# Optimization experiments

Measured on AMD Instinct MI355X. Metric: run time of the kernel, lower is better.

The kernel has to match this reference:

```python
import jax, jax.numpy as jnp
import numpy as np

N, D, S, K = 4096, 256, 32, 4   # nodes, in_dim(=out_dim), subspace_dim, num_heads
ETA = 0.5
LAMBDA_SPARSE = 0.05
EDGE_P = 0.02  # graph density for the random adjacency mask


def setup_inputs() -> dict:
    key = jax.random.key(0)
    k1, k2, k3 = jax.random.split(key, 3)
    H = jax.random.normal(k1, (N, D), dtype=jnp.float32)
    # binary adjacency mask with self-loops, stored as float (matches torch usage)
    mask = (jax.random.uniform(k2, (N, N)) < EDGE_P).astype(jnp.float32)
    adj_mask = jnp.maximum(mask, jnp.eye(N, dtype=jnp.float32))
    # per-head orthonormal subspace bases U[k] = qr(randn(D,S)) -> [K, D, S]
    raw = jax.random.normal(k3, (K, D, S), dtype=jnp.float32)
    U, _ = jnp.linalg.qr(raw)
    log_precision = jnp.zeros((K, S), dtype=jnp.float32)
    threshold = jnp.full((D,), LAMBDA_SPARSE, dtype=jnp.float32)
    return {"H": H, "adj_mask": adj_mask, "U": U,
            "log_precision": log_precision, "threshold": threshold}


def reference(H, adj_mask, U, log_precision, threshold):
    s = U.shape[-1]
    inv_sqrt_s = 1.0 / jnp.sqrt(jnp.asarray(s, dtype=H.dtype))
    neg = (1.0 - adj_mask) * (-1e9)  # [N, N] additive mask

    # scan over heads keeps peak memory at one [N,N] score matrix at a time
    def head_step(agg, xs):
        Uk, lpk = xs                       # [D,S], [S]
        Z = H @ Uk                         # [N,S]  (= Zk^T in the torch code)
        Zs = Z * jnp.exp(lpk)              # precision-scaled
        scores = (Zs @ Z.T) * inv_sqrt_s + neg   # [N,N]
        alpha = jax.nn.softmax(scores, axis=-1)
        agg = agg + (alpha @ Z) @ Uk.T     # [N,D] == (Uk @ (Zk @ alpha^T))^T
        return agg, None

    agg, _ = jax.lax.scan(head_step, jnp.zeros_like(H), (U, log_precision))
    H_half = H + ETA * agg                 # in_dim == out_dim -> no proj

    # soft threshold
    H_out = jnp.sign(H_half) * jax.nn.relu(jnp.abs(H_half) - threshold[None, :])

    # orthogonality loss: sum_k ||Uk^T Uk - I||_F^2 + sum_{k<l} ||Uk^T Ul||_F^2
    C = jnp.einsum('kda,ldb->klab', U, U)  # [K,K,S,S] gram blocks (K,S small)
    Kh = U.shape[0]
    I = jnp.eye(s, dtype=U.dtype)
    diag_blocks = C[jnp.arange(Kh), jnp.arange(Kh)]          # [K,S,S]
    orth_loss = ((diag_blocks - I) ** 2).sum()
    upper = jnp.triu(jnp.ones((Kh, Kh), dtype=U.dtype), 1)[:, :, None, None]
    orth_loss = orth_loss + ((C ** 2) * upper).sum()
    return H_out, orth_loss
```

## Files before the change

kernel.cpp:

```cpp
#include <hip/hip_runtime.h>
#include <math.h>

constexpr int NN = 4096;
constexpr int DD = 256;
constexpr int SS = 32;
constexpr int KK = 4;
constexpr int MAXN = 192;
constexpr int SEGMAX = 96;
constexpr float ETA = 0.5f;
constexpr int RPB = 2;

#define MEMFENCE() __asm__ volatile("" ::: "memory")

typedef float nfloat4 __attribute__((ext_vector_type(4)));
__device__ __forceinline__ float4 ntload4(const float4* p) {
  nfloat4 v = __builtin_nontemporal_load((const nfloat4*)p);
  float4 r; r.x = v.x; r.y = v.y; r.z = v.z; r.w = v.w;
  return r;
}

__global__ __launch_bounds__(256) void prep_kernel(
    const float* __restrict__ H, const float* __restrict__ U,
    const float* __restrict__ lp, float* __restrict__ Z,
    float* __restrict__ elp, float* __restrict__ lossp) {
  __shared__ float Hl[16][DD];
  __shared__ float red[4];
  const int tid = threadIdx.x;

  if (blockIdx.x < 1024) {
    const int k = blockIdx.x & 3;
    const int n0 = (blockIdx.x >> 2) * 16;

    const float4* H4 = (const float4*)(H + (size_t)n0 * DD);
    float4* Hl4 = (float4*)&Hl[0][0];
    for (int i = tid; i < 16 * DD / 4; i += 256) Hl4[i] = H4[i];
    __syncthreads();

    const int s = tid & 31;
    const int n_l = (tid >> 5) & 7;
    const float* Uk = U + (size_t)k * DD * SS;
    float acc0 = 0.f, acc1 = 0.f;
#pragma unroll 4
    for (int dq = 0; dq < DD / 4; dq++) {
      const float4 h0 = Hl4[n_l * (DD / 4) + dq];
      const float4 h1 = Hl4[(n_l + 8) * (DD / 4) + dq];
      const float u0 = Uk[(4 * dq + 0) * SS + s];
      const float u1 = Uk[(4 * dq + 1) * SS + s];
      const float u2 = Uk[(4 * dq + 2) * SS + s];
      const float u3 = Uk[(4 * dq + 3) * SS + s];
      acc0 += h0.x * u0 + h0.y * u1 + h0.z * u2 + h0.w * u3;
      acc1 += h1.x * u0 + h1.y * u1 + h1.z * u2 + h1.w * u3;
    }
    Z[((size_t)k * NN + n0 + n_l) * SS + s] = acc0;
    Z[((size_t)k * NN + n0 + n_l + 8) * SS + s] = acc1;
  } else {
    const int pair = blockIdx.x - 1024;
    if (pair == 0 && tid < KK * SS) elp[tid] = expf(lp[tid]);
    const int pk[10] = {0, 0, 0, 0, 1, 1, 1, 2, 2, 3};
    const int pl[10] = {0, 1, 2, 3, 1, 2, 3, 2, 3, 3};
    const int k = pk[pair], l = pl[pair];
    const int b = tid & 31;
    const int a0 = tid >> 5;
    float4 acc = {0.f, 0.f, 0.f, 0.f};
    const float4* Uk4 = (const float4*)(U + (size_t)k * DD * SS);
    const float* Ul = U + (size_t)l * DD * SS;
    for (int d = 0; d < DD; d++) {
      const float ub = Ul[(size_t)d * SS + b];
      const float4 ua = Uk4[d * (SS / 4) + a0];
      acc.x += ua.x * ub; acc.y += ua.y * ub;
      acc.z += ua.z * ub; acc.w += ua.w * ub;
    }
    const int abase = 4 * a0;
    float cvx = acc.x - ((k == l && abase + 0 == b) ? 1.0f : 0.0f);
    float cvy = acc.y - ((k == l && abase + 1 == b) ? 1.0f : 0.0f);
    float cvz = acc.z - ((k == l && abase + 2 == b) ? 1.0f : 0.0f);
    float cvw = acc.w - ((k == l && abase + 3 == b) ? 1.0f : 0.0f);
    float tot = cvx * cvx + cvy * cvy + cvz * cvz + cvw * cvw;
#pragma unroll
    for (int off = 32; off >= 1; off >>= 1) tot += __shfl_xor(tot, off);
    if ((tid & 63) == 0) red[tid >> 6] = tot;
    __syncthreads();
    if (tid == 0) lossp[pair] = red[0] + red[1] + red[2] + red[3];
  }
}

__global__ __launch_bounds__(256, 8) void attn_epi(
    const float* __restrict__ mask, const float* __restrict__ Z,
    const float* __restrict__ elp, const float* __restrict__ lossp,
    const float* __restrict__ H, const float* __restrict__ U,
    const float* __restrict__ thr, float* __restrict__ Hout,
    float* __restrict__ loss) {
  const int tid = threadIdx.x;
  const int wv = tid >> 6;
  const int lane = tid & 63;
  const int bid = blockIdx.x;

  __shared__ int segn[RPB][4][SEGMAX];
  __shared__ int segc[RPB][4];
  __shared__ int nbr[RPB][MAXN];
  __shared__ float AOl[RPB][KK * SS];

  if (bid == 0 && tid == 0) {
    float t = 0.f;
#pragma unroll
    for (int i = 0; i < 10; i++) t += lossp[i];
    loss[0] = t;
  }

  const unsigned long long lt = (1ULL << lane) - 1ULL;

  {
    const float4* m4 = (const float4*)(mask + (size_t)(bid * RPB) * NN);
    const int base = wv * 256 + lane;
    float4 v[RPB][4];
#pragma unroll
    for (int r = 0; r < RPB; r++)
#pragma unroll
      for (int it = 0; it < 4; it++)
        v[r][it] = ntload4(&m4[(size_t)r * (NN / 4) + base + it * 64]);

#pragma unroll
    for (int r = 0; r < RPB; r++) {
      int cnt = 0;
#pragma unroll
      for (int it = 0; it < 4; it++) {
        const int i = base + it * 64;
        const float4 vv = v[r][it];
        unsigned long long bb;
        bb = __ballot(vv.x > 0.5f);
        if (vv.x > 0.5f) { const int p = cnt + (int)__popcll(bb & lt); if (p < SEGMAX) segn[r][wv][p] = 4 * i; }
        cnt += (int)__popcll(bb);
        bb = __ballot(vv.y > 0.5f);
        if (vv.y > 0.5f) { const int p = cnt + (int)__popcll(bb & lt); if (p < SEGMAX) segn[r][wv][p] = 4 * i + 1; }
        cnt += (int)__popcll(bb);
        bb = __ballot(vv.z > 0.5f);
        if (vv.z > 0.5f) { const int p = cnt + (int)__popcll(bb & lt); if (p < SEGMAX) segn[r][wv][p] = 4 * i + 2; }
        cnt += (int)__popcll(bb);
        bb = __ballot(vv.w > 0.5f);
        if (vv.w > 0.5f) { const int p = cnt + (int)__popcll(bb & lt); if (p < SEGMAX) segn[r][wv][p] = 4 * i + 3; }
        cnt += (int)__popcll(bb);
      }
      if (lane == 0) segc[r][wv] = min(cnt, SEGMAX);
    }
  }
  MEMFENCE();
  __syncthreads();

  int ctot[RPB];
#pragma unroll
  for (int r = 0; r < RPB; r++) {
    const int c0 = segc[r][0], c1 = segc[r][1];
    const int c2 = segc[r][2], c3 = segc[r][3];
    const int offs[4] = {0, c0, c0 + c1, c0 + c1 + c2};
    ctot[r] = min(c0 + c1 + c2 + c3, MAXN);
    const int myc = segc[r][wv];
    const int myoff = offs[wv];
    for (int i = lane; i < myc; i += 64) {
      const int p = myoff + i;
      if (p < MAXN) nbr[r][p] = segn[r][wv][i];
    }
  }
  MEMFENCE();
  __syncthreads();

  const int p_sub = lane >> 3;
  const int sq = lane & 7;
  const float inv_sqrt_s = 0.17677669529663687f;
  const int k = wv;
  const float* Zk = Z + (size_t)k * NN * SS;

#pragma unroll
  for (int r = 0; r < RPB; r++) {
    const int row = bid * RPB + r;
    const int c = ctot[r];
    const int* nb = &nbr[r][0];

    float4 q4;
    {
      const float4 a = ((const float4*)(Z + ((size_t)k * NN + row) * SS))[sq];
      const float4 e = ((const float4*)(elp + k * SS))[sq];
      q4.x = a.x * e.x; q4.y = a.y * e.y; q4.z = a.z * e.z; q4.w = a.w * e.w;
    }

    float m = -3.0e38f;
    float wsum = 0.f;
    float4 o4 = {0.f, 0.f, 0.f, 0.f};

    bool aA = p_sub < c, aB = (p_sub + 8) < c;
    float4 zA = {0.f, 0.f, 0.f, 0.f}, zB = {0.f, 0.f, 0.f, 0.f};
    if (aA) zA = ((const float4*)(Zk + (size_t)nb[p_sub] * SS))[sq];
    if (aB) zB = ((const float4*)(Zk + (size_t)nb[p_sub + 8] * SS))[sq];

    for (int p0 = 0; p0 < c; p0 += 16) {
      const int pa_n = p0 + 16 + p_sub;
      const int pb_n = pa_n + 8;
      const bool aA_n = pa_n < c, aB_n = pb_n < c;
      float4 zA_n = {0.f, 0.f, 0.f, 0.f}, zB_n = {0.f, 0.f, 0.f, 0.f};
      if (aA_n) zA_n = ((const float4*)(Zk + (size_t)nb[pa_n] * SS))[sq];
      if (aB_n) zB_n = ((const float4*)(Zk + (size_t)nb[pb_n] * SS))[sq];

      float dA = q4.x * zA.x + q4.y * zA.y + q4.z * zA.z + q4.w * zA.w;
      float dB = q4.x * zB.x + q4.y * zB.y + q4.z * zB.z + q4.w * zB.w;
      dA += __shfl_xor(dA, 1); dB += __shfl_xor(dB, 1);
      dA += __shfl_xor(dA, 2); dB += __shfl_xor(dB, 2);
      dA += __shfl_xor(dA, 4); dB += __shfl_xor(dB, 4);
      dA = aA ? dA * inv_sqrt_s : -3.0e38f;
      dB = aB ? dB * inv_sqrt_s : -3.0e38f;
      float cm = fmaxf(dA, dB);
      cm = fmaxf(cm, __shfl_xor(cm, 8));
      cm = fmaxf(cm, __shfl_xor(cm, 16));
      cm = fmaxf(cm, __shfl_xor(cm, 32));
      const float mn = fmaxf(m, cm);
      const float sc = __expf(m - mn);
      m = mn;
      const float wA = __expf(dA - m);
      const float wB = __expf(dB - m);
      o4.x = o4.x * sc + wA * zA.x + wB * zB.x;
      o4.y = o4.y * sc + wA * zA.y + wB * zB.y;
      o4.z = o4.z * sc + wA * zA.z + wB * zB.z;
      o4.w = o4.w * sc + wA * zA.w + wB * zB.w;
      wsum = wsum * sc + wA + wB;

      zA = zA_n; zB = zB_n; aA = aA_n; aB = aB_n;
    }
#pragma unroll
    for (int off = 8; off <= 32; off <<= 1) {
      o4.x += __shfl_xor(o4.x, off);
      o4.y += __shfl_xor(o4.y, off);
      o4.z += __shfl_xor(o4.z, off);
      o4.w += __shfl_xor(o4.w, off);
      wsum += __shfl_xor(wsum, off);
    }
    const float invl = 1.0f / wsum;
    if (p_sub == 0) {
      float4 o;
      o.x = o4.x * invl; o.y = o4.y * invl;
      o.z = o4.z * invl; o.w = o4.w * invl;
      ((float4*)&AOl[r][0])[k * 8 + sq] = o;
    }
  }
  MEMFENCE();
  __syncthreads();

  {
    const int r0 = bid * RPB;
    const int d = tid;
    float acc[RPB];
#pragma unroll
    for (int r = 0; r < RPB; r++) acc[r] = 0.f;
    const float4* U4 = (const float4*)U;
    const float4* AOl4 = (const float4*)&AOl[0][0];
#pragma unroll
    for (int kk = 0; kk < KK; kk++) {
      const int ubase = (kk * DD + d) * (SS / 4);
#pragma unroll
      for (int sq2 = 0; sq2 < SS / 4; sq2++) {
        const float4 u = U4[ubase + sq2];
#pragma unroll
        for (int r = 0; r < RPB; r++) {
          const float4 a = AOl4[r * (KK * SS / 4) + kk * (SS / 4) + sq2];
          acc[r] += u.x * a.x + u.y * a.y + u.z * a.z + u.w * a.w;
        }
      }
    }
    const float tv = thr[d];
#pragma unroll
    for (int r = 0; r < RPB; r++) {
      const float h =
          __builtin_nontemporal_load(&H[(size_t)(r0 + r) * DD + d]) + ETA * acc[r];
      const float ab = fabsf(h) - tv;
      const float o = (ab > 0.0f) ? copysignf(ab, h) : 0.0f;
      __builtin_nontemporal_store(o, &Hout[(size_t)(r0 + r) * DD + d]);
    }
  }
}

extern "C" void kernel_launch(void* const* d_in, const int* in_sizes, int n_in,
                              void* d_out, int out_size, void* d_ws, size_t ws_size,
                              hipStream_t stream) {
  const float* H    = (const float*)d_in[0];
  const float* mask = (const float*)d_in[1];
  const float* U    = (const float*)d_in[2];
  const float* lp   = (const float*)d_in[3];
  const float* thr  = (const float*)d_in[4];

  float* Hout = (float*)d_out;
  float* loss = Hout + (size_t)NN * DD;

  float* Z     = (float*)d_ws;
  float* elp   = Z + (size_t)KK * NN * SS;
  float* lossp = elp + KK * SS;

  prep_kernel<<<1034, 256, 0, stream>>>(H, U, lp, Z, elp, lossp);
  attn_epi<<<NN / RPB, 256, 0, stream>>>(mask, Z, elp, lossp, H, U, thr, Hout, loss);
}
```

Before: 175.9 us.

## Move mask compaction into prep kernel and split epilogue across waves with transposed U

The scan of the adjacency mask that builds neighbor lists moves out of the attention kernel into extra blocks of the prep kernel, one wave per row, writing counts and indices to global workspace. That lets the mask streaming overlap with the Z projection and frees the attention kernel from the serial ballot scan. A transposed copy of U is also produced so the epilogue can split work by head across waves with coalesced float4 loads, followed by a shared-memory reduction and a vectorised soft-threshold store. In exchange the neighbor lists make an extra round trip through global memory and the attention kernel gets an added barrier. The launch-bounds occupancy hint of 8 is also dropped.

```diff
diff --git a/kernel.cpp b/kernel.cpp
--- a/kernel.cpp
+++ b/kernel.cpp
@@ -6,9 +6,12 @@
 constexpr int SS = 32;
 constexpr int KK = 4;
 constexpr int MAXN = 192;
-constexpr int SEGMAX = 96;
 constexpr float ETA = 0.5f;
 constexpr int RPB = 2;
+
+constexpr int SCAN0 = 1034;
+constexpr int TRAN0 = 2058;
+constexpr int PREP_GRID = 2074;
 
 #define MEMFENCE() __asm__ volatile("" ::: "memory")
 
@@ -18,18 +21,24 @@
   float4 r; r.x = v.x; r.y = v.y; r.z = v.z; r.w = v.w;
   return r;
 }
+__device__ __forceinline__ void ntstore4(float4* p, float4 v) {
+  nfloat4 t; t.x = v.x; t.y = v.y; t.z = v.z; t.w = v.w;
+  __builtin_nontemporal_store(t, (nfloat4*)p);
+}
 
 __global__ __launch_bounds__(256) void prep_kernel(
     const float* __restrict__ H, const float* __restrict__ U,
-    const float* __restrict__ lp, float* __restrict__ Z,
-    float* __restrict__ elp, float* __restrict__ lossp) {
+    const float* __restrict__ lp, const float* __restrict__ mask,
+    float* __restrict__ Z, float* __restrict__ Ut, float* __restrict__ elp,
+    float* __restrict__ lossp, int* __restrict__ cntg, int* __restrict__ nbrg) {
   __shared__ float Hl[16][DD];
   __shared__ float red[4];
   const int tid = threadIdx.x;
-
-  if (blockIdx.x < 1024) {
-    const int k = blockIdx.x & 3;
-    const int n0 = (blockIdx.x >> 2) * 16;
+  const int bid = blockIdx.x;
+
+  if (bid < 1024) {
+    const int k = bid & 3;
+    const int n0 = (bid >> 2) * 16;
 
     const float4* H4 = (const float4*)(H + (size_t)n0 * DD);
     float4* Hl4 = (float4*)&Hl[0][0];
@@ -53,8 +62,8 @@
     }
     Z[((size_t)k * NN + n0 + n_l) * SS + s] = acc0;
     Z[((size_t)k * NN + n0 + n_l + 8) * SS + s] = acc1;
-  } else {
-    const int pair = blockIdx.x - 1024;
+  } else if (bid < SCAN0) {
+    const int pair = bid - 1024;
     if (pair == 0 && tid < KK * SS) elp[tid] = expf(lp[tid]);
     const int pk[10] = {0, 0, 0, 0, 1, 1, 1, 2, 2, 3};
     const int pl[10] = {0, 1, 2, 3, 1, 2, 3, 2, 3, 3};
@@ -81,24 +90,66 @@
     if ((tid & 63) == 0) red[tid >> 6] = tot;
     __syncthreads();
     if (tid == 0) lossp[pair] = red[0] + red[1] + red[2] + red[3];
-  }
-}
-
-__global__ __launch_bounds__(256, 8) void attn_epi(
-    const float* __restrict__ mask, const float* __restrict__ Z,
-    const float* __restrict__ elp, const float* __restrict__ lossp,
-    const float* __restrict__ H, const float* __restrict__ U,
-    const float* __restrict__ thr, float* __restrict__ Hout,
-    float* __restrict__ loss) {
+  } else if (bid < TRAN0) {
+    const int wv = tid >> 6;
+    const int lane = tid & 63;
+    const int row = (bid - SCAN0) * 4 + wv;
+    const float4* m4 = (const float4*)(mask + (size_t)row * NN);
+    int* ng = nbrg + (size_t)row * MAXN;
+    const unsigned long long lt = (1ULL << lane) - 1ULL;
+    int cnt = 0;
+#pragma unroll
+    for (int bt = 0; bt < 2; bt++) {
+      float4 v[8];
+#pragma unroll
+      for (int j = 0; j < 8; j++)
+        v[j] = ntload4(&m4[(bt * 8 + j) * 64 + lane]);
+#pragma unroll
+      for (int j = 0; j < 8; j++) {
+        const int i = (bt * 8 + j) * 64 + lane;
+        const float4 vv = v[j];
+        unsigned long long bb;
+        bb = __ballot(vv.x > 0.5f);
+        if (vv.x > 0.5f) { const int p = cnt + (int)__popcll(bb & lt); if (p < MAXN) ng[p] = 4 * i; }
+        cnt += (int)__popcll(bb);
+        bb = __ballot(vv.y > 0.5f);
+        if (vv.y > 0.5f) { const int p = cnt + (int)__popcll(bb & lt); if (p < MAXN) ng[p] = 4 * i + 1; }
+        cnt += (int)__popcll(bb);
+        bb = __ballot(vv.z > 0.5f);
+        if (vv.z > 0.5f) { const int p = cnt + (int)__popcll(bb & lt); if (p < MAXN) ng[p] = 4 * i + 2; }
+        cnt += (int)__popcll(bb);
+        bb = __ballot(vv.w > 0.5f);
+        if (vv.w > 0.5f) { const int p = cnt + (int)__popcll(bb & lt); if (p < MAXN) ng[p] = 4 * i + 3; }
+        cnt += (int)__popcll(bb);
+      }
+    }
+    if (lane == 0) cntg[row] = min(cnt, MAXN);
+  } else {
+    const int pair = (bid - TRAN0) * 8 + (tid >> 5);
+    const int k = pair >> 5, s = pair & 31;
+    const int l = tid & 31;
+#pragma unroll
+    for (int j = 0; j < 8; j++) {
+      const int d = l * 8 + j;
+      Ut[(size_t)pair * DD + d] = U[((size_t)k * DD + d) * SS + s];
+    }
+  }
+}
+
+__global__ __launch_bounds__(256) void attn_epi(
+    const int* __restrict__ nbrg, const int* __restrict__ cntg,
+    const float* __restrict__ Z, const float* __restrict__ elp,
+    const float* __restrict__ lossp, const float* __restrict__ H,
+    const float* __restrict__ Ut, const float* __restrict__ thr,
+    float* __restrict__ Hout, float* __restrict__ loss) {
   const int tid = threadIdx.x;
   const int wv = tid >> 6;
   const int lane = tid & 63;
   const int bid = blockIdx.x;
 
-  __shared__ int segn[RPB][4][SEGMAX];
-  __shared__ int segc[RPB][4];
   __shared__ int nbr[RPB][MAXN];
   __shared__ float AOl[RPB][KK * SS];
+  __shared__ float part[RPB][KK][64][4];
 
   if (bid == 0 && tid == 0) {
     float t = 0.f;
@@ -107,59 +158,11 @@
     loss[0] = t;
   }
 
-  const unsigned long long lt = (1ULL << lane) - 1ULL;
-
-  {
-    const float4* m4 = (const float4*)(mask + (size_t)(bid * RPB) * NN);
-    const int base = wv * 256 + lane;
-    float4 v[RPB][4];
-#pragma unroll
-    for (int r = 0; r < RPB; r++)
-#pragma unroll
-      for (int it = 0; it < 4; it++)
-        v[r][it] = ntload4(&m4[(size_t)r * (NN / 4) + base + it * 64]);
-
-#pragma unroll
-    for (int r = 0; r < RPB; r++) {
-      int cnt = 0;
-#pragma unroll
-      for (int it = 0; it < 4; it++) {
-        const int i = base + it * 64;
-        const float4 vv = v[r][it];
-        unsigned long long bb;
-        bb = __ballot(vv.x > 0.5f);
-        if (vv.x > 0.5f) { const int p = cnt + (int)__popcll(bb & lt); if (p < SEGMAX) segn[r][wv][p] = 4 * i; }
-        cnt += (int)__popcll(bb);
-        bb = __ballot(vv.y > 0.5f);
-        if (vv.y > 0.5f) { const int p = cnt + (int)__popcll(bb & lt); if (p < SEGMAX) segn[r][wv][p] = 4 * i + 1; }
-        cnt += (int)__popcll(bb);
-        bb = __ballot(vv.z > 0.5f);
-        if (vv.z > 0.5f) { const int p = cnt + (int)__popcll(bb & lt); if (p < SEGMAX) segn[r][wv][p] = 4 * i + 2; }
-        cnt += (int)__popcll(bb);
-        bb = __ballot(vv.w > 0.5f);
-        if (vv.w > 0.5f) { const int p = cnt + (int)__popcll(bb & lt); if (p < SEGMAX) segn[r][wv][p] = 4 * i + 3; }
-        cnt += (int)__popcll(bb);
-      }
-      if (lane == 0) segc[r][wv] = min(cnt, SEGMAX);
-    }
-  }
-  MEMFENCE();
-  __syncthreads();
-
-  int ctot[RPB];
-#pragma unroll
-  for (int r = 0; r < RPB; r++) {
-    const int c0 = segc[r][0], c1 = segc[r][1];
-    const int c2 = segc[r][2], c3 = segc[r][3];
-    const int offs[4] = {0, c0, c0 + c1, c0 + c1 + c2};
-    ctot[r] = min(c0 + c1 + c2 + c3, MAXN);
-    const int myc = segc[r][wv];
-    const int myoff = offs[wv];
-    for (int i = lane; i < myc; i += 64) {
-      const int p = myoff + i;
-      if (p < MAXN) nbr[r][p] = segn[r][wv][i];
-    }
-  }
+  const int row0 = bid * RPB;
+  const int c0 = cntg[row0];
+  const int c1 = cntg[row0 + 1];
+  if (tid < c0) nbr[0][tid] = nbrg[(size_t)row0 * MAXN + tid];
+  if (tid < c1) nbr[1][tid] = nbrg[(size_t)(row0 + 1) * MAXN + tid];
   MEMFENCE();
   __syncthreads();
 
@@ -171,8 +174,8 @@
 
 #pragma unroll
   for (int r = 0; r < RPB; r++) {
-    const int row = bid * RPB + r;
-    const int c = ctot[r];
+    const int row = row0 + r;
+    const int c = r ? c1 : c0;
     const int* nb = &nbr[r][0];
 
     float4 q4;
@@ -243,35 +246,45 @@
   __syncthreads();
 
   {
-    const int r0 = bid * RPB;
-    const int d = tid;
-    float acc[RPB];
-#pragma unroll
-    for (int r = 0; r < RPB; r++) acc[r] = 0.f;
-    const float4* U4 = (const float4*)U;
-    const float4* AOl4 = (const float4*)&AOl[0][0];
-#pragma unroll
-    for (int kk = 0; kk < KK; kk++) {
-      const int ubase = (kk * DD + d) * (SS / 4);
-#pragma unroll
-      for (int sq2 = 0; sq2 < SS / 4; sq2++) {
-        const float4 u = U4[ubase + sq2];
-#pragma unroll
-        for (int r = 0; r < RPB; r++) {
-          const float4 a = AOl4[r * (KK * SS / 4) + kk * (SS / 4) + sq2];
-          acc[r] += u.x * a.x + u.y * a.y + u.z * a.z + u.w * a.w;
-        }
-      }
-    }
-    const float tv = thr[d];
-#pragma unroll
-    for (int r = 0; r < RPB; r++) {
-      const float h =
-          __builtin_nontemporal_load(&H[(size_t)(r0 + r) * DD + d]) + ETA * acc[r];
-      const float ab = fabsf(h) - tv;
-      const float o = (ab > 0.0f) ? copysignf(ab, h) : 0.0f;
-      __builtin_nontemporal_store(o, &Hout[(size_t)(r0 + r) * DD + d]);
-    }
+    const float4* Ut4 = (const float4*)Ut;
+    float4 acc0 = {0.f, 0.f, 0.f, 0.f};
+    float4 acc1 = {0.f, 0.f, 0.f, 0.f};
+#pragma unroll 8
+    for (int s = 0; s < SS; s++) {
+      const int ks = k * SS + s;
+      const float4 u = Ut4[(size_t)ks * (DD / 4) + lane];
+      const float a0 = AOl[0][ks];
+      const float a1 = AOl[1][ks];
+      acc0.x += a0 * u.x; acc0.y += a0 * u.y; acc0.z += a0 * u.z; acc0.w += a0 * u.w;
+      acc1.x += a1 * u.x; acc1.y += a1 * u.y; acc1.z += a1 * u.z; acc1.w += a1 * u.w;
+    }
+    ((float4*)&part[0][k][lane][0])[0] = acc0;
+    ((float4*)&part[1][k][lane][0])[0] = acc1;
+  }
+  MEMFENCE();
+  __syncthreads();
+
+  if (tid < 64 * RPB) {
+    const int r = tid >> 6;
+    const int l2 = tid & 63;
+    const float4 p0 = ((const float4*)&part[r][0][l2][0])[0];
+    const float4 p1 = ((const float4*)&part[r][1][l2][0])[0];
+    const float4 p2 = ((const float4*)&part[r][2][l2][0])[0];
+    const float4 p3 = ((const float4*)&part[r][3][l2][0])[0];
+    const float4 h4 = ntload4(&((const float4*)(H + (size_t)(row0 + r) * DD))[l2]);
+    const float4 t4 = ((const float4*)thr)[l2];
+    float4 o;
+    const float hx = h4.x + ETA * (p0.x + p1.x + p2.x + p3.x);
+    const float hy = h4.y + ETA * (p0.y + p1.y + p2.y + p3.y);
+    const float hz = h4.z + ETA * (p0.z + p1.z + p2.z + p3.z);
+    const float hw = h4.w + ETA * (p0.w + p1.w + p2.w + p3.w);
+    const float ax = fabsf(hx) - t4.x, ay = fabsf(hy) - t4.y;
+    const float az = fabsf(hz) - t4.z, aw = fabsf(hw) - t4.w;
+    o.x = (ax > 0.f) ? copysignf(ax, hx) : 0.f;
+    o.y = (ay > 0.f) ? copysignf(ay, hy) : 0.f;
+    o.z = (az > 0.f) ? copysignf(az, hz) : 0.f;
+    o.w = (aw > 0.f) ? copysignf(aw, hw) : 0.f;
+    ntstore4(&((float4*)(Hout + (size_t)(row0 + r) * DD))[l2], o);
   }
 }
 
@@ -288,9 +301,14 @@
   float* loss = Hout + (size_t)NN * DD;
 
   float* Z     = (float*)d_ws;
-  float* elp   = Z + (size_t)KK * NN * SS;
+  float* Ut    = Z + (size_t)KK * NN * SS;
+  float* elp   = Ut + (size_t)KK * SS * DD;
   float* lossp = elp + KK * SS;
-
-  prep_kernel<<<1034, 256, 0, stream>>>(H, U, lp, Z, elp, lossp);
-  attn_epi<<<NN / RPB, 256, 0, stream>>>(mask, Z, elp, lossp, H, U, thr, Hout, loss);
-}
+  int*   cntg  = (int*)(lossp + 16);
+  int*   nbrg  = cntg + NN;
+
+  prep_kernel<<<PREP_GRID, 256, 0, stream>>>(H, U, lp, mask, Z, Ut, elp,
+                                             lossp, cntg, nbrg);
+  attn_epi<<<NN / RPB, 256, 0, stream>>>(nbrg, cntg, Z, elp, lossp, H, Ut,
+                                         thr, Hout, loss);
+}
```

New measurement: 150.0 us. 14.7% less time.
